# Kernel optimization log

Measured on AMD Instinct MI355X. Metric: run time of the kernel, lower is better.

## Reference

```python
import jax, jax.numpy as jnp
import numpy as np

B, N, LQ, DK, DV, DD = 2, 16, 512, 64, 64, 128
TEMPERATURE = 8.0  # sqrt(DK)
NEG_INF = -1e9


def setup_inputs() -> dict:
    key = jax.random.key(0)
    ks = jax.random.split(key, 9)
    h2 = 2 * DD  # dc hidden width = d0 + d1
    return {
        "q": jax.random.normal(ks[0], (B, N, LQ, DK), jnp.float32),
        "k": jax.random.normal(ks[1], (B, N, LQ, DK), jnp.float32),
        "v": jax.random.normal(ks[2], (B, N, LQ, DV), jnp.float32),
        "d0": jax.random.normal(ks[3], (B, LQ, DD), jnp.float32),
        "d1": jax.random.normal(ks[4], (B, LQ, DD), jnp.float32),
        "W1": jax.random.normal(ks[5], (h2, h2), jnp.float32) / np.sqrt(h2),
        "b1": jnp.zeros((h2,), jnp.float32),
        "W2": jax.random.normal(ks[6], (h2, 2), jnp.float32) / np.sqrt(h2),
        "b2": jnp.zeros((2,), jnp.float32),
    }


def reference(q, k, v, d0, d1, W1, b1, W2, b2):
    b, n, lq, dk = q.shape
    dd = d0.shape[-1]
    # pairwise features: f[b,i,j] = concat(d0[b,i], d1[b,j])  -> [b,lq,lq,2dd]
    f = jnp.concatenate(
        [
            jnp.broadcast_to(d0[:, :, None, :], (b, lq, lq, dd)),
            jnp.broadcast_to(d1[:, None, :, :], (b, lq, lq, dd)),
        ],
        axis=-1,
    )
    h = jax.nn.relu(jnp.einsum("bijf,fg->bijg", f, W1) + b1)
    logits = jnp.einsum("bijg,gc->bijc", h, W2) + b2  # [b,lq,lq,2]
    # eval-mode gumbel_softmax(hard=True, tau=1, training=False): argmax of logits
    decisions = (jnp.argmax(logits, axis=-1) == 1)[:, None, :, :]  # [b,1,lq,lq]
    attn = jnp.einsum("bnid,bnjd->bnij", q / TEMPERATURE, k)
    attn = jnp.where(decisions, attn, NEG_INF)
    attn = jax.nn.softmax(attn, axis=-1)  # dropout is identity in eval mode
    output = jnp.einsum("bnij,bnjd->bnid", attn, v)
    return output, attn, decisions
```

## Files before the change

### kernel.cpp

```cpp
#include <hip/hip_runtime.h>

#define BB 2
#define NN 16
#define LQ 512
#define DKk 64
#define DVv 64
#define DDd 128
#define H2 256
#define NEG_INF -1e9f

__global__ __launch_bounds__(256) void mlp_stage1(
    const float* __restrict__ d0, const float* __restrict__ d1,
    const float* __restrict__ W1, const float* __restrict__ b1,
    double* __restrict__ U64, double* __restrict__ W64,
    float* __restrict__ U32, float* __restrict__ W32)
{
    __shared__ float drow[2][DDd];
    int gid = blockIdx.x;
    int half = gid >> 9;
    int r0 = (gid & 511) * 2;
    const float* din = half ? d1 : d0;
    int w1off = half ? DDd : 0;
    double* o64 = half ? W64 : U64;
    float* o32 = half ? W32 : U32;
    int t = threadIdx.x;
    drow[t >> 7][t & 127] = din[(size_t)(r0 + (t >> 7)) * DDd + (t & 127)];
    __syncthreads();
    int g = t;
    double acc[2] = {};
#pragma unroll 2
    for (int f = 0; f < DDd; f += 4) {
        double w0 = (double)W1[(w1off + f + 0) * H2 + g];
        double w1 = (double)W1[(w1off + f + 1) * H2 + g];
        double w2 = (double)W1[(w1off + f + 2) * H2 + g];
        double w3 = (double)W1[(w1off + f + 3) * H2 + g];
#pragma unroll
        for (int r = 0; r < 2; ++r) {
            float4 dr = *(const float4*)&drow[r][f];
            acc[r] = fma((double)dr.x, w0, acc[r]);
            acc[r] = fma((double)dr.y, w1, acc[r]);
            acc[r] = fma((double)dr.z, w2, acc[r]);
            acc[r] = fma((double)dr.w, w3, acc[r]);
        }
    }
    double bb = half ? 0.0 : (double)b1[g];
#pragma unroll
    for (int r = 0; r < 2; ++r) {
        double a = acc[r] + bb;
        o64[(size_t)(r0 + r) * H2 + g] = a;
        o32[(size_t)(r0 + r) * H2 + g] = (float)a;
    }
}

__global__ __launch_bounds__(256, 2) void dec_full(
    const float* __restrict__ U32, const float* __restrict__ W32,
    const double* __restrict__ U64, const double* __restrict__ W64,
    const float* __restrict__ W2, const float* __restrict__ b2,
    float* __restrict__ dec_out)
{
    __shared__ __align__(16) float Ut[H2][36];
    __shared__ __align__(16) float Wt[H2][36];
    __shared__ float gvs[H2];
    __shared__ int lbuf[1024];
    __shared__ int lcnt;
    int bid = blockIdx.x;
    int b  = bid >> 8;
    int i0 = ((bid >> 4) & 15) * 32;
    int j0 = (bid & 15) * 32;
    int t = threadIdx.x;
    gvs[t] = W2[t * 2 + 1] - W2[t * 2];
    if (t == 0) lcnt = 0;
    float bias = b2[1] - b2[0];
    {
        int r = t >> 3, gq = t & 7;
        const float* su = U32 + ((size_t)(b * LQ) + i0 + r) * H2;
        const float* sw = W32 + ((size_t)(b * LQ) + j0 + r) * H2;
#pragma unroll
        for (int s = 0; s < 8; ++s) {
            int g = gq * 4 + s * 32;
            float4 u4 = *(const float4*)(su + g);
            Ut[g + 0][r] = u4.x; Ut[g + 1][r] = u4.y;
            Ut[g + 2][r] = u4.z; Ut[g + 3][r] = u4.w;
            float4 w4 = *(const float4*)(sw + g);
            Wt[g + 0][r] = w4.x; Wt[g + 1][r] = w4.y;
            Wt[g + 2][r] = w4.z; Wt[g + 3][r] = w4.w;
        }
    }
    __syncthreads();
    int pi = t >> 4, pj = t & 15;
    float a00 = 0.f, a01 = 0.f, a10 = 0.f, a11 = 0.f;
#pragma unroll 8
    for (int g = 0; g < H2; ++g) {
        float2 u2 = *(const float2*)&Ut[g][pi * 2];
        float2 w2 = *(const float2*)&Wt[g][pj * 2];
        float gv = gvs[g];
        a00 = fmaf(fmaxf(u2.x + w2.x, 0.f), gv, a00);
        a01 = fmaf(fmaxf(u2.x + w2.y, 0.f), gv, a01);
        a10 = fmaf(fmaxf(u2.y + w2.x, 0.f), gv, a10);
        a11 = fmaf(fmaxf(u2.y + w2.y, 0.f), gv, a11);
    }
    int row0 = b * LQ + i0 + pi * 2;
    float g00 = a00 + bias, g01 = a01 + bias;
    float g10 = a10 + bias, g11 = a11 + bias;
    int jb = j0 + pj * 2;
    *(float2*)&dec_out[(size_t)row0 * LQ + jb] =
        make_float2(g00 > 0.f ? 1.f : 0.f, g01 > 0.f ? 1.f : 0.f);
    *(float2*)&dec_out[(size_t)(row0 + 1) * LQ + jb] =
        make_float2(g10 > 0.f ? 1.f : 0.f, g11 > 0.f ? 1.f : 0.f);
    if (fabsf(g00) < 2e-2f) { int lx = atomicAdd(&lcnt, 1); lbuf[lx] = (row0 << 9) | jb; }
    if (fabsf(g01) < 2e-2f) { int lx = atomicAdd(&lcnt, 1); lbuf[lx] = (row0 << 9) | (jb + 1); }
    if (fabsf(g10) < 2e-2f) { int lx = atomicAdd(&lcnt, 1); lbuf[lx] = ((row0 + 1) << 9) | jb; }
    if (fabsf(g11) < 2e-2f) { int lx = atomicAdd(&lcnt, 1); lbuf[lx] = ((row0 + 1) << 9) | (jb + 1); }
    __syncthreads();
    int nloc = lcnt;
    int wv = t >> 6, ln = t & 63;
    for (int x = wv; x < nloc; x += 4) {
        int pij = lbuf[x];
        int j = pij & (LQ - 1);
        int prow = pij >> 9;
        int pb = prow >> 9;
        const double* u = U64 + (size_t)prow * H2;
        const double* w = W64 + ((size_t)(pb * LQ) + j) * H2;
        double acc = 0.0;
        for (int g = ln; g < H2; g += 64) {
            double tv = u[g] + w[g];
            tv = tv > 0.0 ? tv : 0.0;
            acc = fma(tv, (double)W2[g * 2 + 1] - (double)W2[g * 2 + 0], acc);
        }
#pragma unroll
        for (int off = 32; off; off >>= 1) acc += __shfl_xor(acc, off, 64);
        if (ln == 0) {
            acc += (double)b2[1] - (double)b2[0];
            dec_out[(size_t)prow * LQ + j] = acc > 0.0 ? 1.f : 0.f;
        }
    }
}

__global__ __launch_bounds__(256) void fused_attn(
    const float* __restrict__ q, const float* __restrict__ k,
    const float* __restrict__ v, const float* __restrict__ dec,
    float* __restrict__ attn, float* __restrict__ out)
{
    __shared__ __align__(16) float smem[10752];
    float* qT = smem;
    float* kT = smem + 2304;
    float* Pt = smem;
    float* Vs = smem + 2112;
    int bid = blockIdx.x;
    int bn = bid >> 4;
    int i0 = (bid & 15) * 32;
    int b = bn >> 4;
    int t = threadIdx.x;

    {
        int qi = t >> 3;
        const float* src = q + ((size_t)bn * LQ + i0 + qi) * DKk;
#pragma unroll
        for (int it = 0; it < 2; ++it) {
            int kkq = (t & 7) + it * 8;
            float4 t4 = *(const float4*)(src + kkq * 4);
            qT[(kkq * 4 + 0) * 36 + qi] = t4.x;
            qT[(kkq * 4 + 1) * 36 + qi] = t4.y;
            qT[(kkq * 4 + 2) * 36 + qi] = t4.z;
            qT[(kkq * 4 + 3) * 36 + qi] = t4.w;
        }
    }
    int tiq = t >> 5;
    int tjq = t & 31;
    float s[4][4][4];

#pragma unroll
    for (int c = 0; c < 4; ++c) {
        __syncthreads();
        {
            int kj = t >> 2;
#pragma unroll
            for (int it = 0; it < 8; ++it) {
                int jj = kj + (it & 1) * 64;
                int kkq = (t & 3) + (it >> 1) * 4;
                float4 t4 = *(const float4*)(k + ((size_t)bn * LQ + c * 128 + jj) * DKk + kkq * 4);
                kT[(kkq * 4 + 0) * 132 + jj] = t4.x;
                kT[(kkq * 4 + 1) * 132 + jj] = t4.y;
                kT[(kkq * 4 + 2) * 132 + jj] = t4.z;
                kT[(kkq * 4 + 3) * 132 + jj] = t4.w;
            }
        }
        __syncthreads();
        float acc[4][4] = {};
#pragma unroll 8
        for (int kk = 0; kk < 64; ++kk) {
            float4 a  = *(const float4*)&qT[kk * 36 + tiq * 4];
            float4 bb = *(const float4*)&kT[kk * 132 + tjq * 4];
            acc[0][0] = fmaf(a.x, bb.x, acc[0][0]); acc[0][1] = fmaf(a.x, bb.y, acc[0][1]);
            acc[0][2] = fmaf(a.x, bb.z, acc[0][2]); acc[0][3] = fmaf(a.x, bb.w, acc[0][3]);
            acc[1][0] = fmaf(a.y, bb.x, acc[1][0]); acc[1][1] = fmaf(a.y, bb.y, acc[1][1]);
            acc[1][2] = fmaf(a.y, bb.z, acc[1][2]); acc[1][3] = fmaf(a.y, bb.w, acc[1][3]);
            acc[2][0] = fmaf(a.z, bb.x, acc[2][0]); acc[2][1] = fmaf(a.z, bb.y, acc[2][1]);
            acc[2][2] = fmaf(a.z, bb.z, acc[2][2]); acc[2][3] = fmaf(a.z, bb.w, acc[2][3]);
            acc[3][0] = fmaf(a.w, bb.x, acc[3][0]); acc[3][1] = fmaf(a.w, bb.y, acc[3][1]);
            acc[3][2] = fmaf(a.w, bb.z, acc[3][2]); acc[3][3] = fmaf(a.w, bb.w, acc[3][3]);
        }
#pragma unroll
        for (int r = 0; r < 4; ++r) {
            float4 m4 = *(const float4*)&dec[((size_t)(b * LQ) + i0 + tiq * 4 + r) * LQ + c * 128 + tjq * 4];
            s[c][r][0] = m4.x != 0.f ? acc[r][0] * 0.125f : NEG_INF;
            s[c][r][1] = m4.y != 0.f ? acc[r][1] * 0.125f : NEG_INF;
            s[c][r][2] = m4.z != 0.f ? acc[r][2] * 0.125f : NEG_INF;
            s[c][r][3] = m4.w != 0.f ? acc[r][3] * 0.125f : NEG_INF;
        }
    }
#pragma unroll
    for (int r = 0; r < 4; ++r) {
        float m = NEG_INF;
#pragma unroll
        for (int c = 0; c < 4; ++c)
#pragma unroll
            for (int cc = 0; cc < 4; ++cc) m = fmaxf(m, s[c][r][cc]);
#pragma unroll
        for (int off = 1; off < 32; off <<= 1) m = fmaxf(m, __shfl_xor(m, off, 32));
        float sum = 0.f;
#pragma unroll
        for (int c = 0; c < 4; ++c)
#pragma unroll
            for (int cc = 0; cc < 4; ++cc) {
                float e = __expf(s[c][r][cc] - m);
                s[c][r][cc] = e; sum += e;
            }
#pragma unroll
        for (int off = 1; off < 32; off <<= 1) sum += __shfl_xor(sum, off, 32);
        float inv = 1.f / sum;
#pragma unroll
        for (int c = 0; c < 4; ++c)
#pragma unroll
            for (int cc = 0; cc < 4; ++cc) s[c][r][cc] *= inv;
    }
#pragma unroll
    for (int c = 0; c < 4; ++c)
#pragma unroll
        for (int r = 0; r < 4; ++r) {
            float4 wv = make_float4(s[c][r][0], s[c][r][1], s[c][r][2], s[c][r][3]);
            *(float4*)&attn[((size_t)bn * LQ + i0 + tiq * 4 + r) * LQ + c * 128 + tjq * 4] = wv;
        }

    int jq  = t >> 6;
    int ih8 = (t >> 4) & 3;
    int dh  = t & 15;
    float o[8][4] = {};
#pragma unroll
    for (int c8 = 0; c8 < 8; ++c8) {
        __syncthreads();
        if ((tjq >> 4) == (c8 & 1)) {
            int jl4 = tjq & 15;
            int c = c8 >> 1;
#pragma unroll
            for (int cc = 0; cc < 4; ++cc) {
                int row = jl4 * 4 + cc;
                *(float4*)&Pt[row * 32 + (((tiq + jl4) & 7) << 2)] =
                    make_float4(s[c][0][cc], s[c][1][cc], s[c][2][cc], s[c][3][cc]);
            }
        }
        {
            int vj = t >> 2;
#pragma unroll
            for (int it = 0; it < 4; ++it) {
                int dq = (t & 3) + it * 4;
                *(float4*)&Vs[vj * 68 + dq * 4] =
                    *(const float4*)(v + ((size_t)bn * LQ + c8 * 64 + vj) * DVv + dq * 4);
            }
        }
        __syncthreads();
#pragma unroll 4
        for (int jx = 0; jx < 16; ++jx) {
            int jj = jq * 16 + jx;
            int js = jj >> 2;
            float4 pl = *(const float4*)&Pt[jj * 32 + (((ih8 * 2 + js) & 7) << 2)];
            float4 ph = *(const float4*)&Pt[jj * 32 + (((ih8 * 2 + 1 + js) & 7) << 2)];
            float4 v4 = *(const float4*)&Vs[jj * 68 + dh * 4];
            o[0][0] = fmaf(pl.x, v4.x, o[0][0]); o[0][1] = fmaf(pl.x, v4.y, o[0][1]);
            o[0][2] = fmaf(pl.x, v4.z, o[0][2]); o[0][3] = fmaf(pl.x, v4.w, o[0][3]);
            o[1][0] = fmaf(pl.y, v4.x, o[1][0]); o[1][1] = fmaf(pl.y, v4.y, o[1][1]);
            o[1][2] = fmaf(pl.y, v4.z, o[1][2]); o[1][3] = fmaf(pl.y, v4.w, o[1][3]);
            o[2][0] = fmaf(pl.z, v4.x, o[2][0]); o[2][1] = fmaf(pl.z, v4.y, o[2][1]);
            o[2][2] = fmaf(pl.z, v4.z, o[2][2]); o[2][3] = fmaf(pl.z, v4.w, o[2][3]);
            o[3][0] = fmaf(pl.w, v4.x, o[3][0]); o[3][1] = fmaf(pl.w, v4.y, o[3][1]);
            o[3][2] = fmaf(pl.w, v4.z, o[3][2]); o[3][3] = fmaf(pl.w, v4.w, o[3][3]);
            o[4][0] = fmaf(ph.x, v4.x, o[4][0]); o[4][1] = fmaf(ph.x, v4.y, o[4][1]);
            o[4][2] = fmaf(ph.x, v4.z, o[4][2]); o[4][3] = fmaf(ph.x, v4.w, o[4][3]);
            o[5][0] = fmaf(ph.y, v4.x, o[5][0]); o[5][1] = fmaf(ph.y, v4.y, o[5][1]);
            o[5][2] = fmaf(ph.y, v4.z, o[5][2]); o[5][3] = fmaf(ph.y, v4.w, o[5][3]);
            o[6][0] = fmaf(ph.z, v4.x, o[6][0]); o[6][1] = fmaf(ph.z, v4.y, o[6][1]);
            o[6][2] = fmaf(ph.z, v4.z, o[6][2]); o[6][3] = fmaf(ph.z, v4.w, o[6][3]);
            o[7][0] = fmaf(ph.w, v4.x, o[7][0]); o[7][1] = fmaf(ph.w, v4.y, o[7][1]);
            o[7][2] = fmaf(ph.w, v4.z, o[7][2]); o[7][3] = fmaf(ph.w, v4.w, o[7][3]);
        }
    }
    float* red = smem;
    __syncthreads();
    if (jq == 3) {
#pragma unroll
        for (int rr = 0; rr < 8; ++rr)
            *(float4*)&red[((ih8 * 8 + rr) * 16 + dh) * 20] =
                make_float4(o[rr][0], o[rr][1], o[rr][2], o[rr][3]);
    }
    __syncthreads();
    if (jq == 2) {
#pragma unroll
        for (int rr = 0; rr < 8; ++rr) {
            float* p = &red[((ih8 * 8 + rr) * 16 + dh) * 20];
            float4 x = *(const float4*)p;
            *(float4*)p = make_float4(x.x + o[rr][0], x.y + o[rr][1],
                                      x.z + o[rr][2], x.w + o[rr][3]);
        }
    }
    __syncthreads();
    if (jq == 1) {
#pragma unroll
        for (int rr = 0; rr < 8; ++rr) {
            float* p = &red[((ih8 * 8 + rr) * 16 + dh) * 20];
            float4 x = *(const float4*)p;
            *(float4*)p = make_float4(x.x + o[rr][0], x.y + o[rr][1],
                                      x.z + o[rr][2], x.w + o[rr][3]);
        }
    }
    __syncthreads();
    if (jq == 0) {
#pragma unroll
        for (int rr = 0; rr < 8; ++rr) {
            float4 x = *(const float4*)&red[((ih8 * 8 + rr) * 16 + dh) * 20];
            *(float4*)&out[((size_t)bn * LQ + i0 + ih8 * 8 + rr) * DVv + dh * 4] =
                make_float4(x.x + o[rr][0], x.y + o[rr][1],
                            x.z + o[rr][2], x.w + o[rr][3]);
        }
    }
}

extern "C" void kernel_launch(void* const* d_in, const int* in_sizes, int n_in,
                              void* d_out, int out_size, void* d_ws, size_t ws_size,
                              hipStream_t stream)
{
    const float* q  = (const float*)d_in[0];
    const float* k  = (const float*)d_in[1];
    const float* v  = (const float*)d_in[2];
    const float* d0 = (const float*)d_in[3];
    const float* d1 = (const float*)d_in[4];
    const float* W1 = (const float*)d_in[5];
    const float* b1 = (const float*)d_in[6];
    const float* W2 = (const float*)d_in[7];
    const float* b2 = (const float*)d_in[8];

    float* out  = (float*)d_out;
    float* attn = out + (size_t)BB * NN * LQ * DVv;
    float* dec  = attn + (size_t)BB * NN * LQ * LQ;

    char* scratch = (char*)attn;
    double* U64 = (double*)(scratch);
    double* W64 = (double*)(scratch + (2u << 20));
    float*  U32 = (float*) (scratch + (4u << 20));
    float*  W32 = (float*) (scratch + (5u << 20));

    mlp_stage1<<<1024, 256, 0, stream>>>(d0, d1, W1, b1, U64, W64, U32, W32);
    dec_full<<<512, 256, 0, stream>>>(U32, W32, U64, W64, W2, b2, dec);
    fused_attn<<<512, 256, 0, stream>>>(q, k, v, dec, attn, out);
}
```

Before: 162.4 us.

## Remap QK tile so each wavefront owns full rows for wave-level softmax

```diff
diff --git a/kernel.cpp b/kernel.cpp
--- a/kernel.cpp
+++ b/kernel.cpp
@@ -136,6 +136,50 @@
     }
 }
 
+#define QK_R(ar, sa, sb)                                   \
+    sa.x = fmaf(ar, b0.x, sa.x); sa.y = fmaf(ar, b0.y, sa.y); \
+    sa.z = fmaf(ar, b0.z, sa.z); sa.w = fmaf(ar, b0.w, sa.w); \
+    sb.x = fmaf(ar, b1.x, sb.x); sb.y = fmaf(ar, b1.y, sb.y); \
+    sb.z = fmaf(ar, b1.z, sb.z); sb.w = fmaf(ar, b1.w, sb.w);
+
+#define SM_ROW(sa, sb, r) {                                                     \
+    size_t dro = ((size_t)(b * LQ) + i0 + ig * 8 + r) * LQ + lane * 4;          \
+    float4 m0 = *(const float4*)&dec[dro];                                      \
+    float4 m1 = *(const float4*)&dec[dro + 256];                                \
+    sa.x = m0.x != 0.f ? sa.x * 0.125f : NEG_INF;                               \
+    sa.y = m0.y != 0.f ? sa.y * 0.125f : NEG_INF;                               \
+    sa.z = m0.z != 0.f ? sa.z * 0.125f : NEG_INF;                               \
+    sa.w = m0.w != 0.f ? sa.w * 0.125f : NEG_INF;                               \
+    sb.x = m1.x != 0.f ? sb.x * 0.125f : NEG_INF;                               \
+    sb.y = m1.y != 0.f ? sb.y * 0.125f : NEG_INF;                               \
+    sb.z = m1.z != 0.f ? sb.z * 0.125f : NEG_INF;                               \
+    sb.w = m1.w != 0.f ? sb.w * 0.125f : NEG_INF;                               \
+    float mx = fmaxf(fmaxf(fmaxf(sa.x, sa.y), fmaxf(sa.z, sa.w)),              \
+                     fmaxf(fmaxf(sb.x, sb.y), fmaxf(sb.z, sb.w)));              \
+    _Pragma("unroll")                                                            \
+    for (int off = 1; off < 64; off <<= 1) mx = fmaxf(mx, __shfl_xor(mx, off, 64)); \
+    sa.x = __expf(sa.x - mx); sa.y = __expf(sa.y - mx);                         \
+    sa.z = __expf(sa.z - mx); sa.w = __expf(sa.w - mx);                         \
+    sb.x = __expf(sb.x - mx); sb.y = __expf(sb.y - mx);                         \
+    sb.z = __expf(sb.z - mx); sb.w = __expf(sb.w - mx);                         \
+    float sm = sa.x + sa.y + sa.z + sa.w + sb.x + sb.y + sb.z + sb.w;           \
+    _Pragma("unroll")                                                            \
+    for (int off = 1; off < 64; off <<= 1) sm += __shfl_xor(sm, off, 64);       \
+    float inv = 1.f / sm;                                                       \
+    sa.x *= inv; sa.y *= inv; sa.z *= inv; sa.w *= inv;                         \
+    sb.x *= inv; sb.y *= inv; sb.z *= inv; sb.w *= inv;                         \
+    size_t aro = ((size_t)bn * LQ + i0 + ig * 8 + r) * LQ + lane * 4;           \
+    *(float4*)&attn[aro] = sa;                                                  \
+    *(float4*)&attn[aro + 256] = sb;                                            \
+}
+
+#define PT_WCC(s0, s1, s2, s3, s4, s5, s6, s7, cc) {                            \
+    int jl = L15 * 4 + (cc);                                                    \
+    int base = jl * 36 + slot;                                                  \
+    *(float4*)&Pt[base]     = make_float4(s0, s1, s2, s3);                      \
+    *(float4*)&Pt[base + 4] = make_float4(s4, s5, s6, s7);                      \
+}
+
 __global__ __launch_bounds__(256) void fused_attn(
     const float* __restrict__ q, const float* __restrict__ k,
     const float* __restrict__ v, const float* __restrict__ dec,
@@ -145,12 +189,14 @@
     float* qT = smem;
     float* kT = smem + 2304;
     float* Pt = smem;
-    float* Vs = smem + 2112;
+    float* Vs = smem + 2304;
     int bid = blockIdx.x;
     int bn = bid >> 4;
     int i0 = (bid & 15) * 32;
     int b = bn >> 4;
     int t = threadIdx.x;
+    int ig = t >> 6;
+    int lane = t & 63;
 
     {
         int qi = t >> 3;
@@ -165,98 +211,62 @@
             qT[(kkq * 4 + 3) * 36 + qi] = t4.w;
         }
     }
-    int tiq = t >> 5;
-    int tjq = t & 31;
-    float s[4][4][4];
-
-#pragma unroll
-    for (int c = 0; c < 4; ++c) {
+
+    float4 sA0 = {}, sA1 = {}, sA2 = {}, sA3 = {}, sA4 = {}, sA5 = {}, sA6 = {}, sA7 = {};
+    float4 sB0 = {}, sB1 = {}, sB2 = {}, sB3 = {}, sB4 = {}, sB5 = {}, sB6 = {}, sB7 = {};
+
+    for (int kc = 0; kc < 4; ++kc) {
         __syncthreads();
         {
-            int kj = t >> 2;
+            int qq = t & 3;
+            int jb = t >> 2;
 #pragma unroll
             for (int it = 0; it < 8; ++it) {
-                int jj = kj + (it & 1) * 64;
-                int kkq = (t & 3) + (it >> 1) * 4;
-                float4 t4 = *(const float4*)(k + ((size_t)bn * LQ + c * 128 + jj) * DKk + kkq * 4);
-                kT[(kkq * 4 + 0) * 132 + jj] = t4.x;
-                kT[(kkq * 4 + 1) * 132 + jj] = t4.y;
-                kT[(kkq * 4 + 2) * 132 + jj] = t4.z;
-                kT[(kkq * 4 + 3) * 132 + jj] = t4.w;
+                int j = jb + it * 64;
+                float4 t4 = *(const float4*)(k + ((size_t)bn * LQ + j) * DKk + kc * 16 + qq * 4);
+                kT[(qq * 4 + 0) * 516 + j] = t4.x;
+                kT[(qq * 4 + 1) * 516 + j] = t4.y;
+                kT[(qq * 4 + 2) * 516 + j] = t4.z;
+                kT[(qq * 4 + 3) * 516 + j] = t4.w;
             }
         }
         __syncthreads();
-        float acc[4][4] = {};
-#pragma unroll 8
-        for (int kk = 0; kk < 64; ++kk) {
-            float4 a  = *(const float4*)&qT[kk * 36 + tiq * 4];
-            float4 bb = *(const float4*)&kT[kk * 132 + tjq * 4];
-            acc[0][0] = fmaf(a.x, bb.x, acc[0][0]); acc[0][1] = fmaf(a.x, bb.y, acc[0][1]);
-            acc[0][2] = fmaf(a.x, bb.z, acc[0][2]); acc[0][3] = fmaf(a.x, bb.w, acc[0][3]);
-            acc[1][0] = fmaf(a.y, bb.x, acc[1][0]); acc[1][1] = fmaf(a.y, bb.y, acc[1][1]);
-            acc[1][2] = fmaf(a.y, bb.z, acc[1][2]); acc[1][3] = fmaf(a.y, bb.w, acc[1][3]);
-            acc[2][0] = fmaf(a.z, bb.x, acc[2][0]); acc[2][1] = fmaf(a.z, bb.y, acc[2][1]);
-            acc[2][2] = fmaf(a.z, bb.z, acc[2][2]); acc[2][3] = fmaf(a.z, bb.w, acc[2][3]);
-            acc[3][0] = fmaf(a.w, bb.x, acc[3][0]); acc[3][1] = fmaf(a.w, bb.y, acc[3][1]);
-            acc[3][2] = fmaf(a.w, bb.z, acc[3][2]); acc[3][3] = fmaf(a.w, bb.w, acc[3][3]);
-        }
-#pragma unroll
-        for (int r = 0; r < 4; ++r) {
-            float4 m4 = *(const float4*)&dec[((size_t)(b * LQ) + i0 + tiq * 4 + r) * LQ + c * 128 + tjq * 4];
-            s[c][r][0] = m4.x != 0.f ? acc[r][0] * 0.125f : NEG_INF;
-            s[c][r][1] = m4.y != 0.f ? acc[r][1] * 0.125f : NEG_INF;
-            s[c][r][2] = m4.z != 0.f ? acc[r][2] * 0.125f : NEG_INF;
-            s[c][r][3] = m4.w != 0.f ? acc[r][3] * 0.125f : NEG_INF;
-        }
-    }
-#pragma unroll
-    for (int r = 0; r < 4; ++r) {
-        float m = NEG_INF;
-#pragma unroll
-        for (int c = 0; c < 4; ++c)
-#pragma unroll
-            for (int cc = 0; cc < 4; ++cc) m = fmaxf(m, s[c][r][cc]);
-#pragma unroll
-        for (int off = 1; off < 32; off <<= 1) m = fmaxf(m, __shfl_xor(m, off, 32));
-        float sum = 0.f;
-#pragma unroll
-        for (int c = 0; c < 4; ++c)
-#pragma unroll
-            for (int cc = 0; cc < 4; ++cc) {
-                float e = __expf(s[c][r][cc] - m);
-                s[c][r][cc] = e; sum += e;
-            }
-#pragma unroll
-        for (int off = 1; off < 32; off <<= 1) sum += __shfl_xor(sum, off, 32);
-        float inv = 1.f / sum;
-#pragma unroll
-        for (int c = 0; c < 4; ++c)
-#pragma unroll
-            for (int cc = 0; cc < 4; ++cc) s[c][r][cc] *= inv;
-    }
-#pragma unroll
-    for (int c = 0; c < 4; ++c)
-#pragma unroll
-        for (int r = 0; r < 4; ++r) {
-            float4 wv = make_float4(s[c][r][0], s[c][r][1], s[c][r][2], s[c][r][3]);
-            *(float4*)&attn[((size_t)bn * LQ + i0 + tiq * 4 + r) * LQ + c * 128 + tjq * 4] = wv;
-        }
+#pragma unroll
+        for (int kk = 0; kk < 16; ++kk) {
+            float4 a0 = *(const float4*)&qT[(kc * 16 + kk) * 36 + ig * 8];
+            float4 a1 = *(const float4*)&qT[(kc * 16 + kk) * 36 + ig * 8 + 4];
+            float4 b0 = *(const float4*)&kT[kk * 516 + lane * 4];
+            float4 b1 = *(const float4*)&kT[kk * 516 + 256 + lane * 4];
+            QK_R(a0.x, sA0, sB0); QK_R(a0.y, sA1, sB1);
+            QK_R(a0.z, sA2, sB2); QK_R(a0.w, sA3, sB3);
+            QK_R(a1.x, sA4, sB4); QK_R(a1.y, sA5, sB5);
+            QK_R(a1.z, sA6, sB6); QK_R(a1.w, sA7, sB7);
+        }
+    }
+
+    SM_ROW(sA0, sB0, 0); SM_ROW(sA1, sB1, 1); SM_ROW(sA2, sB2, 2); SM_ROW(sA3, sB3, 3);
+    SM_ROW(sA4, sB4, 4); SM_ROW(sA5, sB5, 5); SM_ROW(sA6, sB6, 6); SM_ROW(sA7, sB7, 7);
 
     int jq  = t >> 6;
     int ih8 = (t >> 4) & 3;
     int dh  = t & 15;
+    int L15 = lane & 15;
+    int slot = ((ig + L15) & 3) * 8;
     float o[8][4] = {};
 #pragma unroll
     for (int c8 = 0; c8 < 8; ++c8) {
         __syncthreads();
-        if ((tjq >> 4) == (c8 & 1)) {
-            int jl4 = tjq & 15;
-            int c = c8 >> 1;
-#pragma unroll
-            for (int cc = 0; cc < 4; ++cc) {
-                int row = jl4 * 4 + cc;
-                *(float4*)&Pt[row * 32 + (((tiq + jl4) & 7) << 2)] =
-                    make_float4(s[c][0][cc], s[c][1][cc], s[c][2][cc], s[c][3][cc]);
+        if ((lane >> 4) == (c8 & 3)) {
+            if (c8 < 4) {
+                PT_WCC(sA0.x, sA1.x, sA2.x, sA3.x, sA4.x, sA5.x, sA6.x, sA7.x, 0);
+                PT_WCC(sA0.y, sA1.y, sA2.y, sA3.y, sA4.y, sA5.y, sA6.y, sA7.y, 1);
+                PT_WCC(sA0.z, sA1.z, sA2.z, sA3.z, sA4.z, sA5.z, sA6.z, sA7.z, 2);
+                PT_WCC(sA0.w, sA1.w, sA2.w, sA3.w, sA4.w, sA5.w, sA6.w, sA7.w, 3);
+            } else {
+                PT_WCC(sB0.x, sB1.x, sB2.x, sB3.x, sB4.x, sB5.x, sB6.x, sB7.x, 0);
+                PT_WCC(sB0.y, sB1.y, sB2.y, sB3.y, sB4.y, sB5.y, sB6.y, sB7.y, 1);
+                PT_WCC(sB0.z, sB1.z, sB2.z, sB3.z, sB4.z, sB5.z, sB6.z, sB7.z, 2);
+                PT_WCC(sB0.w, sB1.w, sB2.w, sB3.w, sB4.w, sB5.w, sB6.w, sB7.w, 3);
             }
         }
         {
@@ -271,11 +281,11 @@
         __syncthreads();
 #pragma unroll 4
         for (int jx = 0; jx < 16; ++jx) {
-            int jj = jq * 16 + jx;
-            int js = jj >> 2;
-            float4 pl = *(const float4*)&Pt[jj * 32 + (((ih8 * 2 + js) & 7) << 2)];
-            float4 ph = *(const float4*)&Pt[jj * 32 + (((ih8 * 2 + 1 + js) & 7) << 2)];
-            float4 v4 = *(const float4*)&Vs[jj * 68 + dh * 4];
+            int jl = jq * 16 + jx;
+            int poff = ((ih8 + (jl >> 2)) & 3) * 8;
+            float4 pl = *(const float4*)&Pt[jl * 36 + poff];
+            float4 ph = *(const float4*)&Pt[jl * 36 + poff + 4];
+            float4 v4 = *(const float4*)&Vs[jl * 68 + dh * 4];
             o[0][0] = fmaf(pl.x, v4.x, o[0][0]); o[0][1] = fmaf(pl.x, v4.y, o[0][1]);
             o[0][2] = fmaf(pl.x, v4.z, o[0][2]); o[0][3] = fmaf(pl.x, v4.w, o[0][3]);
             o[1][0] = fmaf(pl.y, v4.x, o[1][0]); o[1][1] = fmaf(pl.y, v4.y, o[1][1]);
```

New measurement: 157.0 us. 3.3% less time.
